# Kernel optimization log

Measured on AMD Instinct MI355X. Metric: run time of the kernel, lower is better.

## Reference

```python
import jax, jax.numpy as jnp
import numpy as np
import math

B = 2; SEQ = 4096; D_MODEL = 768; D_STATE = 128; D_CONV = 4; EXPAND = 2; HEAD_DIM = 64
D_INNER = EXPAND * D_MODEL; D_SSM = D_INNER; NH = D_SSM // HEAD_DIM  # 24 heads
CONV_DIM = D_SSM + 2 * D_STATE; CHUNK = 256
D_IN_PROJ = 2 * D_INNER + 2 * D_STATE + NH


def causal_conv1d(x, w, b):
    # x: [B, C, L]; w: [C, W] depthwise kernel; left-pad for causality; silu activation
    W = w.shape[-1]; L = x.shape[-1]
    xp = jnp.pad(x, ((0, 0), (0, 0), (W - 1, 0)))
    y = b[None, :, None] + sum(xp[:, :, k:k + L] * w[None, :, k, None] for k in range(W))
    return jax.nn.silu(y)


def segsum(a):
    # a: [..., S] -> [..., S, S]; entry (i,j) = sum_{k=j+1..i} a_k for i>=j, -inf above diag
    S = a.shape[-1]
    cs = jnp.cumsum(a, -1)
    d = cs[..., :, None] - cs[..., None, :]
    mask = jnp.tril(jnp.ones((S, S), bool))
    return jnp.where(mask, d, -jnp.inf)


def ssd_chunk_scan(x, dt, A, Bm, Cm, Dp, chunk):
    # Mamba2 SSD chunked selective scan. x:[b,l,h,p] dt:[b,l,h] A:[h] Bm,Cm:[b,l,n] Dp:[h]
    b, l, h, p = x.shape; n = Bm.shape[-1]; nc = l // chunk
    xc = x.reshape(b, nc, chunk, h, p)
    Bc = Bm.reshape(b, nc, chunk, n)
    Cc = Cm.reshape(b, nc, chunk, n)
    dtc = dt.reshape(b, nc, chunk, h)
    a = jnp.transpose(A[None, None, None, :] * dtc, (0, 3, 1, 2))  # [b,h,c,s]
    Acs = jnp.cumsum(a, -1)
    Lm = jnp.exp(segsum(a))  # [b,h,c,s,s] lower-triangular decay
    # intra-chunk (diagonal block) outputs
    Ydiag = jnp.einsum('bcsn,bczn,bhcsz,bczh,bczhp->bcshp', Cc, Bc, Lm, dtc, xc)
    # per-chunk end states
    decay_states = jnp.exp(Acs[..., -1:] - Acs)  # [b,h,c,s]
    states = jnp.einsum('bczn,bhcz,bczh,bczhp->bchpn', Bc, decay_states, dtc, xc)
    # inter-chunk recurrence over nc chunks (small) via scan
    decay_chunk = jnp.exp(Acs[..., -1])  # [b,h,c]
    def step(hcar, inp):
        dcy, st = inp
        return dcy[..., None, None] * hcar + st, hcar  # emit state entering chunk
    _, prev = jax.lax.scan(step, jnp.zeros_like(states[:, 0]),
                           (jnp.moveaxis(decay_chunk, -1, 0), jnp.moveaxis(states, 1, 0)))
    prev = jnp.moveaxis(prev, 0, 1)  # [b,c,h,p,n]
    Yoff = jnp.einsum('bcsn,bchpn,bhcs->bcshp', Cc, prev, jnp.exp(Acs))
    return (Ydiag + Yoff).reshape(b, l, h, p) + Dp[None, None, :, None] * x


def _forward(u, time_diff, W_in, b_in, conv_w, conv_b, tconv1_w, tconv1_b,
             tconv2_w, tconv2_b, mlp_w1, mlp_b1, mlp_w2, mlp_b2, gate_w, gate_b,
             ln_w, ln_b, A_log, dt_bias, Dp, norm_w, W_out, b_out):
    silu = jax.nn.silu
    zxbcdt = u @ W_in.T + b_in  # [B,L,d_in_proj], d_mlp=0
    z = zxbcdt[..., :D_SSM]
    xBC = zxbcdt[..., D_SSM:D_SSM + CONV_DIM]
    dt = zxbcdt[..., D_SSM + CONV_DIM:]  # [B,L,H]
    A = -jnp.exp(A_log)
    xBC = jnp.transpose(causal_conv1d(jnp.transpose(xBC, (0, 2, 1)), conv_w, conv_b), (0, 2, 1))
    # time-gated dt path (time_diff: [B,H,L])
    ts = silu(time_diff @ mlp_w1.T + mlp_b1) @ mlp_w2.T + mlp_b2
    tdt = ts * time_diff
    tdt = causal_conv1d(tdt, tconv1_w, tconv1_b)
    tdt = causal_conv1d(tdt, tconv2_w, tconv2_b)  # [B,H,L]
    final_dt = dt * jnp.transpose(tdt, (0, 2, 1))
    x = xBC[..., :D_SSM]
    Bm = xBC[..., D_SSM:D_SSM + D_STATE]
    Cm = xBC[..., D_SSM + D_STATE:]
    dt_sp = jax.nn.softplus(final_dt + dt_bias)
    xh = x.reshape(x.shape[0], x.shape[1], NH, HEAD_DIM)
    y = ssd_chunk_scan(xh, dt_sp, A, Bm, Cm, Dp, CHUNK).reshape(x.shape[0], x.shape[1], D_SSM)
    # gated RMSNorm (norm_before_gate=False): gate first, then normalize
    yg = y * silu(z)
    y = yg * jax.lax.rsqrt(jnp.mean(yg * yg, -1, keepdims=True) + 1e-12) * norm_w
    out = y @ W_out.T + b_out
    # time residual gate + LayerNorm over seq_len
    tg = jax.nn.sigmoid(time_diff @ gate_w.T + gate_b)  # [B,H,1]
    tmix = tg * time_diff + (1.0 - tg) * tdt
    mu = jnp.mean(tmix, -1, keepdims=True)
    var = jnp.mean((tmix - mu) ** 2, -1, keepdims=True)
    time_out = (tmix - mu) * jax.lax.rsqrt(var + 1e-12) * ln_w + ln_b
    return out, time_out


def setup_inputs():
    key = jax.random.key(0)
    ks = jax.random.split(key, 16)
    def nrm(k, shape, scale=0.02):
        return jax.random.normal(k, shape, jnp.float32) * scale
    dtv = jnp.exp(jax.random.uniform(ks[10], (NH,), jnp.float32) * (math.log(0.1) - math.log(0.001)) + math.log(0.001))
    dtv = jnp.clip(dtv, 1e-4)
    dt_bias = dtv + jnp.log(-jnp.expm1(-dtv))
    A_log = jnp.log(jax.random.uniform(ks[11], (NH,), jnp.float32, 1.0, 16.0))
    return dict(
        u=jax.random.normal(ks[0], (B, SEQ, D_MODEL), jnp.float32),
        time_diff=jax.random.uniform(ks[1], (B, NH, SEQ), jnp.float32),
        W_in=nrm(ks[2], (D_IN_PROJ, D_MODEL)), b_in=jnp.zeros((D_IN_PROJ,), jnp.float32),
        conv_w=nrm(ks[3], (CONV_DIM, D_CONV), 0.2), conv_b=jnp.zeros((CONV_DIM,), jnp.float32),
        tconv1_w=nrm(ks[4], (NH, D_CONV), 0.2), tconv1_b=jnp.zeros((NH,), jnp.float32),
        tconv2_w=nrm(ks[5], (NH, D_CONV), 0.2), tconv2_b=jnp.zeros((NH,), jnp.float32),
        mlp_w1=nrm(ks[6], (SEQ, SEQ)), mlp_b1=jnp.zeros((SEQ,), jnp.float32),
        mlp_w2=nrm(ks[7], (SEQ, SEQ)), mlp_b2=jnp.zeros((SEQ,), jnp.float32),
        gate_w=nrm(ks[8], (1, SEQ)), gate_b=jnp.zeros((1,), jnp.float32),
        ln_w=jnp.ones((SEQ,), jnp.float32), ln_b=jnp.zeros((SEQ,), jnp.float32),
        A_log=A_log, dt_bias=dt_bias, Dp=jnp.ones((NH,), jnp.float32),
        norm_w=jnp.ones((D_SSM,), jnp.float32),
        W_out=nrm(ks[9], (D_MODEL, D_INNER)), b_out=jnp.zeros((D_MODEL,), jnp.float32),
    )


def reference(u, time_diff, W_in, b_in, conv_w, conv_b, tconv1_w, tconv1_b,
              tconv2_w, tconv2_b, mlp_w1, mlp_b1, mlp_w2, mlp_b2, gate_w, gate_b,
              ln_w, ln_b, A_log, dt_bias, Dp, norm_w, W_out, b_out):
    return _forward(u, time_diff, W_in, b_in, conv_w, conv_b, tconv1_w, tconv1_b,
                    tconv2_w, tconv2_b, mlp_w1, mlp_b1, mlp_w2, mlp_b2, gate_w, gate_b,
                    ln_w, ln_b, A_log, dt_bias, Dp, norm_w, W_out, b_out)
```

## Files before the change

### kernel.cpp

```cpp
#include <hip/hip_runtime.h>
#include <math.h>

#define BB 2
#define SEQ 4096
#define DMODEL 768
#define DSTATE 128
#define NHH 24
#define HDIM 64
#define DSSM 1536
#define CDIM 1792
#define CHK 256
#define NC 16
#define DPROJ 3352
#define MR (BB*SEQ)
#define KSPLIT 32
#define XSTR 1920
#define CT 16
#define SXS 270
#define STS 134

typedef __attribute__((ext_vector_type(8))) short bf16x8;
typedef __attribute__((ext_vector_type(8))) unsigned short u16x8;
typedef __attribute__((ext_vector_type(4))) float f32x4;

__device__ __forceinline__ float siluf(float x) { return x / (1.0f + expf(-x)); }

__device__ __forceinline__ unsigned short f2bf(float f) {
    unsigned u = __float_as_uint(f);
    unsigned r = (u + 0x7fffu + ((u >> 16) & 1u)) >> 16;
    return (unsigned short)r;
}

__device__ __forceinline__ float bf2f(unsigned short u) {
    return __uint_as_float(((unsigned)u) << 16);
}

__device__ __forceinline__ float4 bf2f4(ushort4 v) {
    float4 o;
    o.x = bf2f(v.x); o.y = bf2f(v.y); o.z = bf2f(v.z); o.w = bf2f(v.w);
    return o;
}

__device__ __forceinline__ bf16x8 pack8(float4 a, float4 b) {
    u16x8 r;
    r[0] = f2bf(a.x); r[1] = f2bf(a.y); r[2] = f2bf(a.z); r[3] = f2bf(a.w);
    r[4] = f2bf(b.x); r[5] = f2bf(b.y); r[6] = f2bf(b.z); r[7] = f2bf(b.w);
    return *(bf16x8*)&r;
}

__device__ __forceinline__ void gload_lds16(const void* g, void* l) {
    __builtin_amdgcn_global_load_lds((const __attribute__((address_space(1))) unsigned int*)g,
                                     (__attribute__((address_space(3))) unsigned int*)l, 16, 0, 0);
}

__global__ __launch_bounds__(256) void cvt_bf16_k(const float* __restrict__ in,
    unsigned short* __restrict__ out, int n_valid, int n_total)
{
    int i = (blockIdx.x * 256 + threadIdx.x) * 4;
    if (i >= n_total) return;
    ushort4 o;
    if (i + 3 < n_valid) {
        float4 v = *(const float4*)&in[i];
        o.x = f2bf(v.x); o.y = f2bf(v.y); o.z = f2bf(v.z); o.w = f2bf(v.w);
    } else {
        o.x = (i + 0 < n_valid) ? f2bf(in[i + 0]) : 0;
        o.y = (i + 1 < n_valid) ? f2bf(in[i + 1]) : 0;
        o.z = (i + 2 < n_valid) ? f2bf(in[i + 2]) : 0;
        o.w = (i + 3 < n_valid) ? f2bf(in[i + 3]) : 0;
    }
    *(ushort4*)&out[i] = o;
}

__global__ __launch_bounds__(256) void gemm_mfma_dual(
    const unsigned short* __restrict__ A,
    const unsigned short* __restrict__ B1, const float* __restrict__ bias1,
    unsigned short* __restrict__ C1, int N1, int NT1, int nbias1, int NWG1,
    const unsigned short* __restrict__ B2, const float* __restrict__ bias2,
    unsigned short* __restrict__ C2, int N2, int NT2, int nbias2,
    int K, int KT)
{
    __shared__ unsigned short SMEM[24576];
    const int tid = threadIdx.x;
    const int w = tid >> 6, l = tid & 63;
    const int wr = w >> 1, wc = w & 1;
    const int lr = l & 15, lk = l >> 4;
    const int lkx = lk ^ ((lr >> 1) & 3);
    int nwg = gridDim.x, bid = blockIdx.x;
    int wg = (nwg & 7) ? bid : ((bid & 7) * (nwg >> 3) + (bid >> 3));
    const unsigned short* B;
    const float* bias;
    unsigned short* C;
    int N, NT, nbias;
    if (wg < NWG1) { B = B1; bias = bias1; C = C1; N = N1; NT = NT1; nbias = nbias1; }
    else { wg -= NWG1; B = B2; bias = bias2; C = C2; N = N2; NT = NT2; nbias = nbias2; }
    const int m0 = (wg / NT) * 128, n0 = (wg % NT) * 128;
    f32x4 acc[4][4] = {};
    const int i16 = w * 64 + l;
    const int row0 = i16 >> 2, sl = i16 & 3;
    const int slx = sl ^ ((row0 >> 1) & 3);
    const size_t ga0 = (size_t)(m0 + row0) * K + slx * 8;
    const size_t ga1 = (size_t)(m0 + row0 + 64) * K + slx * 8;
    const size_t gb0 = (size_t)(n0 + row0) * K + slx * 8;
    const size_t gb1 = (size_t)(n0 + row0 + 64) * K + slx * 8;
    const int lo0 = (w * 64) * 8;
    const int lo1 = (256 + w * 64) * 8;

#define STAGE(bb, kt) { int ko = (kt) * 32; int bs = (bb) * 8192;            \
      gload_lds16(A + ga0 + ko, &SMEM[bs + lo0]);                            \
      gload_lds16(A + ga1 + ko, &SMEM[bs + lo1]);                            \
      gload_lds16(B + gb0 + ko, &SMEM[bs + 4096 + lo0]);                     \
      gload_lds16(B + gb1 + ko, &SMEM[bs + 4096 + lo1]); }

    STAGE(0, 0);
    STAGE(1, 1);
    for (int kt = 0; kt < KT; ++kt) {
        if (kt + 1 < KT) {
            asm volatile("s_waitcnt vmcnt(4)" ::: "memory");
        } else {
            asm volatile("s_waitcnt vmcnt(0)" ::: "memory");
        }
        __builtin_amdgcn_s_barrier();
        if (kt + 2 < KT) STAGE((kt + 2) % 3, kt + 2);
        int bs = (kt % 3) * 8192;
        bf16x8 af[4], bg[4];
#pragma unroll
        for (int mi = 0; mi < 4; ++mi)
            af[mi] = *(const bf16x8*)&SMEM[bs + (wr * 64 + mi * 16 + lr) * 32 + lkx * 8];
#pragma unroll
        for (int nj = 0; nj < 4; ++nj)
            bg[nj] = *(const bf16x8*)&SMEM[bs + 4096 + (wc * 64 + nj * 16 + lr) * 32 + lkx * 8];
#pragma unroll
        for (int mi = 0; mi < 4; ++mi)
#pragma unroll
            for (int nj = 0; nj < 4; ++nj)
                acc[mi][nj] = __builtin_amdgcn_mfma_f32_16x16x32_bf16(af[mi], bg[nj], acc[mi][nj], 0, 0, 0);
    }
#undef STAGE
    {
        unsigned short* CL = SMEM;
#pragma unroll
        for (int half = 0; half < 2; ++half) {
            __syncthreads();
            if (wr == half) {
#pragma unroll
                for (int nj = 0; nj < 4; ++nj) {
                    int col = n0 + wc * 64 + nj * 16 + lr;
                    float bz = (col < nbias) ? bias[col] : 0.f;
                    int cl = wc * 64 + nj * 16 + lr;
#pragma unroll
                    for (int mi = 0; mi < 4; ++mi)
#pragma unroll
                        for (int r = 0; r < 4; ++r)
                            CL[(mi * 16 + lk * 4 + r) * 136 + cl] = f2bf(acc[mi][nj][r] + bz);
                }
            }
            __syncthreads();
            for (int i = tid; i < 1024; i += 256) {
                int rr = i >> 4, c8 = (i & 15) * 8;
                int m = m0 + half * 64 + rr;
                *(u16x8*)&C[(size_t)m * N + n0 + c8] = *(const u16x8*)&CL[rr * 136 + c8];
            }
        }
    }
}

__global__ __launch_bounds__(256) void gemm_skinny_mfma(const float* __restrict__ A,
    const float* __restrict__ Bw, float* __restrict__ part, int N, int K)
{
    const int nb = blockIdx.x, kb = blockIdx.y;
    const int n0 = nb * 128;
    const int KS = K / KSPLIT;
    const int k0 = kb * KS;
    const int tid = threadIdx.x;
    const int w = tid >> 6, l = tid & 63;
    const int lr = l & 15, lk = l >> 4;
    const int nw0 = n0 + w * 32;
    f32x4 acc[3][2] = {};
    for (int kt = 0; kt < KS; kt += 32) {
        int kk = k0 + kt + lk * 8;
        bf16x8 af[3], bfr[2];
#pragma unroll
        for (int mi = 0; mi < 3; ++mi) {
            const float* ap = &A[(size_t)(mi * 16 + lr) * K + kk];
            af[mi] = pack8(*(const float4*)ap, *(const float4*)(ap + 4));
        }
#pragma unroll
        for (int nf = 0; nf < 2; ++nf) {
            const float* bp = &Bw[(size_t)(nw0 + nf * 16 + lr) * K + kk];
            bfr[nf] = pack8(*(const float4*)bp, *(const float4*)(bp + 4));
        }
#pragma unroll
        for (int mi = 0; mi < 3; ++mi)
#pragma unroll
            for (int nf = 0; nf < 2; ++nf)
                acc[mi][nf] = __builtin_amdgcn_mfma_f32_16x16x32_bf16(af[mi], bfr[nf], acc[mi][nf], 0, 0, 0);
    }
    float* pb = part + (size_t)kb * 48 * N;
#pragma unroll
    for (int mi = 0; mi < 3; ++mi)
#pragma unroll
        for (int r = 0; r < 4; ++r)
#pragma unroll
            for (int nf = 0; nf < 2; ++nf)
                pb[(size_t)(mi * 16 + lk * 4 + r) * N + nw0 + nf * 16 + lr] = acc[mi][nf][r];
}

__global__ __launch_bounds__(256) void conv_xbc_k(const unsigned short* __restrict__ xbc,
    const float* __restrict__ cw, const float* __restrict__ cb,
    unsigned short* __restrict__ out)
{
    int idx = blockIdx.x * 256 + threadIdx.x;
    if (idx >= 448 * (MR / CT)) return;
    int slot = idx % 448;
    int g = idx / 448;
    int c4 = slot * 4;
    int b = g / (SEQ / CT);
    int t0 = (g % (SEQ / CT)) * CT;
    size_t rb = (size_t)b * SEQ;
    float4 cw0 = *(const float4*)&cw[(c4 + 0) * 4];
    float4 cw1 = *(const float4*)&cw[(c4 + 1) * 4];
    float4 cw2 = *(const float4*)&cw[(c4 + 2) * 4];
    float4 cw3 = *(const float4*)&cw[(c4 + 3) * 4];
    float4 cbv = *(const float4*)&cb[c4];
    float4 zero = {0.f, 0.f, 0.f, 0.f};
    float4 w0, w1, w2;
    w0 = (t0 - 3 >= 0) ? bf2f4(*(const ushort4*)&xbc[(rb + t0 - 3) * XSTR + c4]) : zero;
    w1 = (t0 - 2 >= 0) ? bf2f4(*(const ushort4*)&xbc[(rb + t0 - 2) * XSTR + c4]) : zero;
    w2 = (t0 - 1 >= 0) ? bf2f4(*(const ushort4*)&xbc[(rb + t0 - 1) * XSTR + c4]) : zero;
#pragma unroll
    for (int i = 0; i < CT; ++i) {
        int t = t0 + i;
        float4 w3 = bf2f4(*(const ushort4*)&xbc[(rb + t) * XSTR + c4]);
        float a0 = cbv.x + w0.x * cw0.x + w1.x * cw0.y + w2.x * cw0.z + w3.x * cw0.w;
        float a1 = cbv.y + w0.y * cw1.x + w1.y * cw1.y + w2.y * cw1.z + w3.y * cw1.w;
        float a2 = cbv.z + w0.z * cw2.x + w1.z * cw2.y + w2.z * cw2.z + w3.z * cw2.w;
        float a3 = cbv.w + w0.w * cw3.x + w1.w * cw3.y + w2.w * cw3.z + w3.w * cw3.w;
        ushort4 o;
        o.x = f2bf(siluf(a0)); o.y = f2bf(siluf(a1));
        o.z = f2bf(siluf(a2)); o.w = f2bf(siluf(a3));
        *(ushort4*)&out[(rb + t) * CDIM + c4] = o;
        w0 = w1; w1 = w2; w2 = w3;
    }
}

__global__ __launch_bounds__(256) void reduce_part_k(const float* __restrict__ part,
    const float* __restrict__ bias, float* __restrict__ out, int N, int act)
{
    int idx = blockIdx.x * 256 + threadIdx.x;
    if (idx >= 48 * N) return;
    int n = idx % N;
    float s = bias[n];
#pragma unroll
    for (int kb = 0; kb < KSPLIT; ++kb) s += part[(size_t)kb * 48 * N + idx];
    if (act) s = siluf(s);
    out[idx] = s;
}

__global__ __launch_bounds__(256) void time_conv_k(const float* __restrict__ ts,
    const float* __restrict__ td, const float* __restrict__ w1, const float* __restrict__ b1,
    const float* __restrict__ w2, const float* __restrict__ b2, float* __restrict__ tdt)
{
    __shared__ float u0[SEQ];
    __shared__ float u1[SEQ];
    int row = blockIdx.x, h = row % NHH;
    const float* tsr = ts + (size_t)row * SEQ;
    const float* tdr = td + (size_t)row * SEQ;
    for (int i = threadIdx.x; i < SEQ; i += 256) u0[i] = tsr[i] * tdr[i];
    __syncthreads();
    float wa[4], wb[4];
#pragma unroll
    for (int k = 0; k < 4; ++k) { wa[k] = w1[h * 4 + k]; wb[k] = w2[h * 4 + k]; }
    float ba = b1[h], bbv = b2[h];
    for (int i = threadIdx.x; i < SEQ; i += 256) {
        float acc = ba;
#pragma unroll
        for (int k = 0; k < 4; ++k) { int tt = i + k - 3; if (tt >= 0) acc = fmaf(u0[tt], wa[k], acc); }
        u1[i] = siluf(acc);
    }
    __syncthreads();
    for (int i = threadIdx.x; i < SEQ; i += 256) {
        float acc = bbv;
#pragma unroll
        for (int k = 0; k < 4; ++k) { int tt = i + k - 3; if (tt >= 0) acc = fmaf(u1[tt], wb[k], acc); }
        tdt[(size_t)row * SEQ + i] = siluf(acc);
    }
}

__global__ __launch_bounds__(256) void dtsp_cum_k(const unsigned short* __restrict__ r1,
    const float* __restrict__ tdt, const float* __restrict__ dt_bias,
    const float* __restrict__ A_log, float* __restrict__ dtp, float* __restrict__ acs)
{
    __shared__ float wsum[4];
    int blk = blockIdx.x;
    int c = blk % NC;
    int bh = blk / NC;
    int h = bh % NHH, b = bh / NHH;
    int tid = threadIdx.x;
    int s = c * CHK + tid;
    size_t base = (size_t)bh * SEQ + s;
    float x = bf2f(r1[((size_t)(b * SEQ + s)) * XSTR + CDIM + h]) * tdt[base] + dt_bias[h];
    float dt = (x > 20.0f) ? x : log1pf(expf(x));
    dtp[base] = dt;
    float Ah = -expf(A_log[h]);
    float v = Ah * dt;
    int ln = tid & 63;
#pragma unroll
    for (int off = 1; off < 64; off <<= 1) {
        float t = __shfl_up(v, off, 64);
        if (ln >= off) v += t;
    }
    if (ln == 63) wsum[tid >> 6] = v;
    __syncthreads();
    float add = 0.f;
    int wv = tid >> 6;
#pragma unroll
    for (int i = 0; i < 3; ++i)
        if (i < wv) add += wsum[i];
    acs[base] = v + add;
}

__global__ __launch_bounds__(256) void ssd_states_sraw_k(const unsigned short* __restrict__ xc,
    const float* __restrict__ dtp, const float* __restrict__ acs_g,
    float* __restrict__ st, unsigned short* __restrict__ sraw)
{
    __shared__ float s_coef[256];
    __shared__ unsigned short SXT[64 * STS];
    __shared__ unsigned short SBT[128 * STS];
    int bid = blockIdx.x;
    int blk = (gridDim.x & 7) ? bid : ((bid & 7) * (gridDim.x >> 3) + (bid >> 3));
    int tid = threadIdx.x;
    int w = tid >> 6, l = tid & 63;
    int lr = l & 15, lk = l >> 4;
    if (blk >= BB * NC * NHH) {
        int t = blk - BB * NC * NHH;
        int bc = t / 10, tile = t % 10;
        int rem = tile, st_i = 0;
        for (st_i = 0; ; ++st_i) { if (rem < st_i + 1) break; rem -= st_i + 1; }
        int zt = rem;
        int b = bc / NC, c = bc % NC;
        size_t rowbase = (size_t)b * SEQ + c * CHK;
        for (int i = tid; i < 64 * 32; i += 256) {
            int r = i >> 5, c4 = (i & 31) * 4;
            *(ushort4*)&SXT[r * STS + c4] = *(const ushort4*)&xc[(rowbase + st_i * 64 + r) * CDIM + DSSM + DSTATE + c4];
            *(ushort4*)&SBT[r * STS + c4] = *(const ushort4*)&xc[(rowbase + zt * 64 + r) * CDIM + DSSM + c4];
        }
        __syncthreads();
        f32x4 d[4] = {};
#pragma unroll
        for (int kt = 0; kt < 4; ++kt) {
            bf16x8 av = *(const bf16x8*)&SXT[(w * 16 + lr) * STS + kt * 32 + lk * 8];
            bf16x8 bv[4];
#pragma unroll
            for (int nj = 0; nj < 4; ++nj)
                bv[nj] = *(const bf16x8*)&SBT[(nj * 16 + lr) * STS + kt * 32 + lk * 8];
#pragma unroll
            for (int nj = 0; nj < 4; ++nj)
                d[nj] = __builtin_amdgcn_mfma_f32_16x16x32_bf16(av, bv[nj], d[nj], 0, 0, 0);
        }
        unsigned short* tp = sraw + (size_t)bc * 16 * 4096 + (size_t)(st_i * 4 + zt) * 4096;
#pragma unroll
        for (int nj = 0; nj < 4; ++nj)
#pragma unroll
            for (int r = 0; r < 4; ++r)
                tp[(w * 16 + lk * 4 + r) * 64 + nj * 16 + lr] = f2bf(d[nj][r]);
        return;
    }
    int h = blk % NHH, c = (blk / NHH) % NC, b = blk / (NHH * NC);
    size_t rowbase = (size_t)b * SEQ + c * CHK;
    size_t dbase = (size_t)(b * NHH + h) * SEQ + c * CHK;
    float alv = acs_g[dbase + 255];
    s_coef[tid] = expf(alv - acs_g[dbase + tid]) * dtp[dbase + tid];
    __syncthreads();
    f32x4 acc[4][2] = {};
    for (int z0 = 0; z0 < CHK; z0 += 128) {
        if (z0) __syncthreads();
        for (int i = tid; i < 128 * 8; i += 256) {
            int zz = i >> 3, p8 = (i & 7) * 8;
            float sc = s_coef[z0 + zz];
            u16x8 v = *(const u16x8*)&xc[(rowbase + z0 + zz) * CDIM + h * HDIM + p8];
#pragma unroll
            for (int e = 0; e < 8; ++e)
                SXT[(p8 + e) * STS + zz] = f2bf(bf2f(v[e]) * sc);
        }
        for (int i = tid; i < 128 * 16; i += 256) {
            int zz = i >> 4, n8 = (i & 15) * 8;
            u16x8 v = *(const u16x8*)&xc[(rowbase + z0 + zz) * CDIM + DSSM + n8];
#pragma unroll
            for (int e = 0; e < 8; ++e)
                SBT[(n8 + e) * STS + zz] = v[e];
        }
        __syncthreads();
#pragma unroll
        for (int kt = 0; kt < 4; ++kt) {
            bf16x8 av[4], bv[2];
#pragma unroll
            for (int mi = 0; mi < 4; ++mi)
                av[mi] = *(const bf16x8*)&SXT[(mi * 16 + lr) * STS + kt * 32 + lk * 8];
#pragma unroll
            for (int nj = 0; nj < 2; ++nj)
                bv[nj] = *(const bf16x8*)&SBT[(w * 32 + nj * 16 + lr) * STS + kt * 32 + lk * 8];
#pragma unroll
            for (int mi = 0; mi < 4; ++mi)
#pragma unroll
                for (int nj = 0; nj < 2; ++nj)
                    acc[mi][nj] = __builtin_amdgcn_mfma_f32_16x16x32_bf16(av[mi], bv[nj], acc[mi][nj], 0, 0, 0);
        }
    }
    size_t base = (size_t)blk * (HDIM * DSTATE);
#pragma unroll
    for (int mi = 0; mi < 4; ++mi)
#pragma unroll
        for (int r = 0; r < 4; ++r) {
            int p = mi * 16 + lk * 4 + r;
#pragma unroll
            for (int nj = 0; nj < 2; ++nj)
                st[base + p * DSTATE + w * 32 + nj * 16 + lr] = acc[mi][nj][r];
        }
}

__global__ __launch_bounds__(256) void ssd_scan_k(const float* __restrict__ st,
    const float* __restrict__ acs_g, unsigned short* __restrict__ pv16)
{
    int b = blockIdx.x / NHH, h = blockIdx.x % NHH;
    int tid = threadIdx.x;
    float carry[32];
#pragma unroll
    for (int j = 0; j < 32; ++j) carry[j] = 0.f;
    for (int c = 0; c < NC; ++c) {
        int bch = (b * NC + c) * NHH + h;
        size_t base = (size_t)bch * (HDIM * DSTATE);
        float dcy = expf(acs_g[(size_t)(b * NHH + h) * SEQ + c * CHK + 255]);
#pragma unroll
        for (int j = 0; j < 32; ++j) {
            pv16[base + tid + j * 256] = f2bf(carry[j]);
            carry[j] = fmaf(dcy, carry[j], st[base + tid + j * 256]);
        }
    }
}

__global__ __launch_bounds__(256) void ssd_y2_k(const unsigned short* __restrict__ xc,
    const float* __restrict__ dtp, const float* __restrict__ acs_g,
    const unsigned short* __restrict__ sraw, const unsigned short* __restrict__ pv16,
    const float* __restrict__ Dp, unsigned short* __restrict__ Ybf)
{
    __shared__ unsigned short SXT[32 * SXS];
    int bid = blockIdx.x;
    int blk2 = (gridDim.x & 7) ? bid : ((bid & 7) * (gridDim.x >> 3) + (bid >> 3));
    int half = blk2 & 1;
    int blk = blk2 >> 1;
    int h = blk % NHH;
    int c = (blk / NHH) % NC;
    int b = blk / (NHH * NC);
    int tid = threadIdx.x;
    int w = tid >> 6, l = tid & 63;
    int lr = l & 15, lk = l >> 4;
    int pbase = half * 32;
    size_t rowbase = (size_t)b * SEQ + c * CHK;
    size_t dbase = (size_t)(b * NHH + h) * SEQ + c * CHK;
    for (int i = tid; i < 256 * 4; i += 256) {
        int z = i >> 2, p8 = (i & 3) * 8;
        float az0q = acs_g[dbase + (z & 192)];
        float e = az0q - acs_g[dbase + z];
        if (e > 60.f) e = 60.f;
        float sc = expf(e) * dtp[dbase + z];
        u16x8 v = *(const u16x8*)&xc[(rowbase + z) * CDIM + h * HDIM + pbase + p8];
#pragma unroll
        for (int e2 = 0; e2 < 8; ++e2)
            SXT[(p8 + e2) * SXS + z] = f2bf(bf2f(v[e2]) * sc);
    }
    float az0w = acs_g[dbase + w * 64];
    float esw[4][4];
#pragma unroll
    for (int mi = 0; mi < 4; ++mi)
#pragma unroll
        for (int r = 0; r < 4; ++r)
            esw[mi][r] = expf(acs_g[dbase + w * 64 + mi * 16 + lk * 4 + r] - az0w);
    __syncthreads();

    const unsigned short* tbase = sraw + (size_t)(b * NC + c) * 16 * 4096;
    const unsigned short* pvbase = pv16 + (size_t)blk * (HDIM * DSTATE);
    f32x4 acc[4][2] = {};
    for (int zt = 0; zt < w; ++zt) {
        const unsigned short* tp = tbase + (size_t)(w * 4 + zt) * 4096;
        f32x4 tmp[4][2] = {};
#pragma unroll
        for (int kt = 0; kt < 2; ++kt) {
            bf16x8 av[4], bv[2];
#pragma unroll
            for (int mi = 0; mi < 4; ++mi)
                av[mi] = *(const bf16x8*)&tp[(mi * 16 + lr) * 64 + kt * 32 + lk * 8];
#pragma unroll
            for (int nj = 0; nj < 2; ++nj)
                bv[nj] = *(const bf16x8*)&SXT[(nj * 16 + lr) * SXS + zt * 64 + kt * 32 + lk * 8];
#pragma unroll
            for (int mi = 0; mi < 4; ++mi)
#pragma unroll
                for (int nj = 0; nj < 2; ++nj)
                    tmp[mi][nj] = __builtin_amdgcn_mfma_f32_16x16x32_bf16(av[mi], bv[nj], tmp[mi][nj], 0, 0, 0);
        }
        float rho = expf(az0w - acs_g[dbase + zt * 64]);
#pragma unroll
        for (int mi = 0; mi < 4; ++mi)
#pragma unroll
            for (int r = 0; r < 4; ++r) {
                float es = esw[mi][r] * rho;
#pragma unroll
                for (int nj = 0; nj < 2; ++nj)
                    acc[mi][nj][r] += es * tmp[mi][nj][r];
            }
    }
    {
        const unsigned short* tp = tbase + (size_t)(w * 4 + w) * 4096;
        f32x4 tmp[4][2] = {};
#pragma unroll
        for (int kt = 0; kt < 2; ++kt) {
            bf16x8 av[4], bv[2];
#pragma unroll
            for (int mi = 0; mi < 4; ++mi) {
                av[mi] = *(const bf16x8*)&tp[(mi * 16 + lr) * 64 + kt * 32 + lk * 8];
                int zb = kt * 32 + lk * 8;
                int sl = mi * 16 + lr;
#pragma unroll
                for (int e = 0; e < 8; ++e)
                    if (zb + e > sl) av[mi][e] = 0;
            }
#pragma unroll
            for (int nj = 0; nj < 2; ++nj)
                bv[nj] = *(const bf16x8*)&SXT[(nj * 16 + lr) * SXS + w * 64 + kt * 32 + lk * 8];
#pragma unroll
            for (int mi = 0; mi < 4; ++mi)
#pragma unroll
                for (int nj = 0; nj < 2; ++nj)
                    tmp[mi][nj] = __builtin_amdgcn_mfma_f32_16x16x32_bf16(av[mi], bv[nj], tmp[mi][nj], 0, 0, 0);
        }
#pragma unroll
        for (int mi = 0; mi < 4; ++mi)
#pragma unroll
            for (int r = 0; r < 4; ++r) {
                float es = esw[mi][r];
#pragma unroll
                for (int nj = 0; nj < 2; ++nj)
                    acc[mi][nj][r] += es * tmp[mi][nj][r];
            }
    }
    {
        f32x4 tmp[4][2] = {};
#pragma unroll
        for (int kt = 0; kt < 4; ++kt) {
            bf16x8 av[4], bv[2];
#pragma unroll
            for (int mi = 0; mi < 4; ++mi)
                av[mi] = *(const bf16x8*)&xc[(rowbase + w * 64 + mi * 16 + lr) * CDIM + DSSM + DSTATE + kt * 32 + lk * 8];
#pragma unroll
            for (int nj = 0; nj < 2; ++nj)
                bv[nj] = *(const bf16x8*)&pvbase[(pbase + nj * 16 + lr) * DSTATE + kt * 32 + lk * 8];
#pragma unroll
            for (int mi = 0; mi < 4; ++mi)
#pragma unroll
                for (int nj = 0; nj < 2; ++nj)
                    tmp[mi][nj] = __builtin_amdgcn_mfma_f32_16x16x32_bf16(av[mi], bv[nj], tmp[mi][nj], 0, 0, 0);
        }
        float eoff = expf(az0w);
#pragma unroll
        for (int mi = 0; mi < 4; ++mi)
#pragma unroll
            for (int r = 0; r < 4; ++r) {
                float es = esw[mi][r] * eoff;
#pragma unroll
                for (int nj = 0; nj < 2; ++nj)
                    acc[mi][nj][r] += es * tmp[mi][nj][r];
            }
    }
    float dph = Dp[h];
#pragma unroll
    for (int mi = 0; mi < 4; ++mi) {
#pragma unroll
        for (int r = 0; r < 4; ++r) {
            int s = w * 64 + mi * 16 + lk * 4 + r;
#pragma unroll
            for (int nj = 0; nj < 2; ++nj) {
                int p = pbase + nj * 16 + lr;
                float xv = bf2f(xc[(rowbase + s) * CDIM + h * HDIM + p]);
                Ybf[(rowbase + s) * DSSM + h * HDIM + p] = f2bf(acc[mi][nj][r] + dph * xv);
            }
        }
    }
}

__global__ __launch_bounds__(256) void rmsnorm_k(const unsigned short* __restrict__ Ybf_in,
    const unsigned short* __restrict__ zbf, const float* __restrict__ nw,
    unsigned short* __restrict__ Ybf_out)
{
    __shared__ float red[8];
    int row = blockIdx.x;
    const unsigned short* y = Ybf_in + (size_t)row * DSSM;
    const unsigned short* z = zbf + (size_t)row * DSSM;
    float v[6];
    float ss = 0.f;
#pragma unroll
    for (int k = 0; k < 6; ++k) {
        int i = threadIdx.x + k * 256;
        float g = bf2f(y[i]) * siluf(bf2f(z[i]));
        v[k] = g;
        ss = fmaf(g, g, ss);
    }
#pragma unroll
    for (int o = 32; o > 0; o >>= 1) ss += __shfl_down(ss, o, 64);
    int wv = threadIdx.x >> 6, ln = threadIdx.x & 63;
    if (ln == 0) red[wv] = ss;
    __syncthreads();
    float tot = red[0] + red[1] + red[2] + red[3];
    float sc = rsqrtf(tot / (float)DSSM + 1e-12f);
    unsigned short* yo = Ybf_out + (size_t)row * DSSM;
#pragma unroll
    for (int k = 0; k < 6; ++k) {
        int i = threadIdx.x + k * 256;
        yo[i] = f2bf(v[k] * sc * nw[i]);
    }
}

__global__ __launch_bounds__(256) void gemm_out_timeout_k(
    const unsigned short* __restrict__ A, const unsigned short* __restrict__ B,
    const float* __restrict__ bias, float* __restrict__ C, int N, int K, int KT, int NT, int NWGG,
    const float* __restrict__ td, const float* __restrict__ tdt,
    const float* __restrict__ gw, const float* __restrict__ gb,
    const float* __restrict__ lnw, const float* __restrict__ lnb, float* __restrict__ out2)
{
    __shared__ __align__(16) unsigned char SMEMRAW[49152];
    unsigned short* SMEM = (unsigned short*)SMEMRAW;
    const int tid = threadIdx.x;
    int nwg = gridDim.x, bid = blockIdx.x;
    int wg = (nwg & 7) ? bid : ((bid & 7) * (nwg >> 3) + (bid >> 3));
    if (wg >= NWGG) {
        float* tm = (float*)SMEMRAW;
        __shared__ float red[8];
        int row = wg - NWGG;
        const float* tdr = td + (size_t)row * SEQ;
        const float* tdtr = tdt + (size_t)row * SEQ;
        int wv = tid >> 6, ln = tid & 63;
        float part = 0.f;
        for (int i = tid; i < SEQ; i += 256) part = fmaf(tdr[i], gw[i], part);
#pragma unroll
        for (int o = 32; o > 0; o >>= 1) part += __shfl_down(part, o, 64);
        if (ln == 0) red[wv] = part;
        __syncthreads();
        float dot = red[0] + red[1] + red[2] + red[3];
        float tg = 1.f / (1.f + expf(-(dot + gb[0])));
        __syncthreads();
        float sum = 0.f;
        for (int i = tid; i < SEQ; i += 256) {
            float x = tg * tdr[i] + (1.f - tg) * tdtr[i];
            tm[i] = x;
            sum += x;
        }
#pragma unroll
        for (int o = 32; o > 0; o >>= 1) sum += __shfl_down(sum, o, 64);
        if (ln == 0) red[wv] = sum;
        __syncthreads();
        float mu = (red[0] + red[1] + red[2] + red[3]) / (float)SEQ;
        __syncthreads();
        float s2 = 0.f;
        for (int i = tid; i < SEQ; i += 256) { float d = tm[i] - mu; s2 = fmaf(d, d, s2); }
#pragma unroll
        for (int o = 32; o > 0; o >>= 1) s2 += __shfl_down(s2, o, 64);
        if (ln == 0) red[wv] = s2;
        __syncthreads();
        float var = (red[0] + red[1] + red[2] + red[3]) / (float)SEQ;
        float inv = rsqrtf(var + 1e-12f);
        for (int i = tid; i < SEQ; i += 256)
            out2[(size_t)row * SEQ + i] = (tm[i] - mu) * inv * lnw[i] + lnb[i];
        return;
    }
    const int w = tid >> 6, l = tid & 63;
    const int wr = w >> 1, wc = w & 1;
    const int lr = l & 15, lk = l >> 4;
    const int lkx = lk ^ ((lr >> 1) & 3);
    const int m0 = (wg / NT) * 128, n0 = (wg % NT) * 128;
    f32x4 acc[4][4] = {};
    const int i16 = w * 64 + l;
    const int row0 = i16 >> 2, sl = i16 & 3;
    const int slx = sl ^ ((row0 >> 1) & 3);
    const size_t ga0 = (size_t)(m0 + row0) * K + slx * 8;
    const size_t ga1 = (size_t)(m0 + row0 + 64) * K + slx * 8;
    const size_t gb0 = (size_t)(n0 + row0) * K + slx * 8;
    const size_t gb1 = (size_t)(n0 + row0 + 64) * K + slx * 8;
    const int lo0 = (w * 64) * 8;
    const int lo1 = (256 + w * 64) * 8;

#define STAGE3(bb, kt) { int ko = (kt) * 32; int bs = (bb) * 8192;           \
      gload_lds16(A + ga0 + ko, &SMEM[bs + lo0]);                            \
      gload_lds16(A + ga1 + ko, &SMEM[bs + lo1]);                            \
      gload_lds16(B + gb0 + ko, &SMEM[bs + 4096 + lo0]);                     \
      gload_lds16(B + gb1 + ko, &SMEM[bs + 4096 + lo1]); }

    STAGE3(0, 0);
    STAGE3(1, 1);
    for (int kt = 0; kt < KT; ++kt) {
        if (kt + 1 < KT) {
            asm volatile("s_waitcnt vmcnt(4)" ::: "memory");
        } else {
            asm volatile("s_waitcnt vmcnt(0)" ::: "memory");
        }
        __builtin_amdgcn_s_barrier();
        if (kt + 2 < KT) STAGE3((kt + 2) % 3, kt + 2);
        int bs = (kt % 3) * 8192;
        bf16x8 af[4], bg[4];
#pragma unroll
        for (int mi = 0; mi < 4; ++mi)
            af[mi] = *(const bf16x8*)&SMEM[bs + (wr * 64 + mi * 16 + lr) * 32 + lkx * 8];
#pragma unroll
        for (int nj = 0; nj < 4; ++nj)
            bg[nj] = *(const bf16x8*)&SMEM[bs + 4096 + (wc * 64 + nj * 16 + lr) * 32 + lkx * 8];
#pragma unroll
        for (int mi = 0; mi < 4; ++mi)
#pragma unroll
            for (int nj = 0; nj < 4; ++nj)
                acc[mi][nj] = __builtin_amdgcn_mfma_f32_16x16x32_bf16(af[mi], bg[nj], acc[mi][nj], 0, 0, 0);
    }
#undef STAGE3
#pragma unroll
    for (int nj = 0; nj < 4; ++nj) {
        int col = n0 + wc * 64 + nj * 16 + lr;
        float bz = bias[col];
#pragma unroll
        for (int mi = 0; mi < 4; ++mi) {
#pragma unroll
            for (int r = 0; r < 4; ++r) {
                int m = m0 + wr * 64 + mi * 16 + lk * 4 + r;
                C[(size_t)m * N + col] = acc[mi][nj][r] + bz;
            }
        }
    }
}

extern "C" void kernel_launch(void* const* d_in, const int* in_sizes, int n_in,
                              void* d_out, int out_size, void* d_ws, size_t ws_size,
                              hipStream_t stream)
{
    const float* u      = (const float*)d_in[0];
    const float* td     = (const float*)d_in[1];
    const float* W_in   = (const float*)d_in[2];
    const float* b_in   = (const float*)d_in[3];
    const float* conv_w = (const float*)d_in[4];
    const float* conv_b = (const float*)d_in[5];
    const float* t1w    = (const float*)d_in[6];
    const float* t1b    = (const float*)d_in[7];
    const float* t2w    = (const float*)d_in[8];
    const float* t2b    = (const float*)d_in[9];
    const float* m1w    = (const float*)d_in[10];
    const float* m1b    = (const float*)d_in[11];
    const float* m2w    = (const float*)d_in[12];
    const float* m2b    = (const float*)d_in[13];
    const float* gw     = (const float*)d_in[14];
    const float* gb     = (const float*)d_in[15];
    const float* lnw    = (const float*)d_in[16];
    const float* lnb    = (const float*)d_in[17];
    const float* A_log  = (const float*)d_in[18];
    const float* dt_bias= (const float*)d_in[19];
    const float* Dpv    = (const float*)d_in[20];
    const float* nw     = (const float*)d_in[21];
    const float* W_out  = (const float*)d_in[22];
    const float* b_out  = (const float*)d_in[23];
    float* out  = (float*)d_out;
    float* out2 = out + (size_t)MR * DMODEL;

    float* ws = (float*)d_ws;
    size_t o = 0;
    float* zbuf  = ws + o; o += (size_t)MR * DSSM;
    float* r1    = ws + o; o += (size_t)MR * DSSM;
    float* xcv   = ws + o; o += (size_t)MR * CDIM / 2;
    float* partb = ws + o; o += (size_t)KSPLIT * 48 * SEQ;
    float* hid   = ws + o; o += (size_t)BB * NHH * SEQ;
    float* tss   = ws + o; o += (size_t)BB * NHH * SEQ;
    float* tdt   = ws + o; o += (size_t)BB * NHH * SEQ;
    float* dtp   = ws + o; o += (size_t)MR * NHH;
    float* acs_g = ws + o; o += (size_t)MR * NHH;
    float* pvb   = ws + o; o += (size_t)BB * NC * NHH * HDIM * DSTATE;
    unsigned short* sraw = (unsigned short*)(ws + o); o += (size_t)BB * NC * 16 * 4096 / 2;
    unsigned short* r1b = (unsigned short*)r1;
    float* stb = r1;
    unsigned short* ybf16 = (unsigned short*)r1;
    unsigned short* xcv_bf = (unsigned short*)xcv;
    unsigned short* u_bf  = (unsigned short*)pvb;
    unsigned short* Wi_bf = (unsigned short*)(pvb + 3145728);
    unsigned short* pv16  = (unsigned short*)pvb;
    unsigned short* zbf   = (unsigned short*)zbuf;
    unsigned short* Y_bf  = (unsigned short*)xcv;
    unsigned short* Wo_bf = (unsigned short*)(zbuf + 6291456);

    dim3 blk(256);
    const int NWG1 = (XSTR / 128) * (MR / 128);

    cvt_bf16_k<<<dim3((MR * DMODEL / 4 + 255) / 256), blk, 0, stream>>>(u, u_bf, MR * DMODEL, MR * DMODEL);
    cvt_bf16_k<<<dim3((3456 * DMODEL / 4 + 255) / 256), blk, 0, stream>>>(W_in, Wi_bf, DPROJ * DMODEL, 3456 * DMODEL);
    cvt_bf16_k<<<dim3((DMODEL * DSSM / 4 + 255) / 256), blk, 0, stream>>>(W_out, Wo_bf, DMODEL * DSSM, DMODEL * DSSM);
    gemm_skinny_mfma<<<dim3(SEQ / 128, KSPLIT), blk, 0, stream>>>(td, m1w, partb, SEQ, SEQ);
    gemm_mfma_dual<<<dim3(NWG1 + (DSSM / 128) * (MR / 128)), blk, 0, stream>>>(
        u_bf,
        Wi_bf + (size_t)DSSM * DMODEL, b_in + DSSM, r1b, XSTR, XSTR / 128, DPROJ - DSSM, NWG1,
        Wi_bf, b_in, zbf, DSSM, DSSM / 128, DSSM,
        DMODEL, DMODEL / 32);
    reduce_part_k<<<dim3((48 * SEQ + 255) / 256), blk, 0, stream>>>(partb, m1b, hid, SEQ, 1);
    gemm_skinny_mfma<<<dim3(SEQ / 128, KSPLIT), blk, 0, stream>>>(hid, m2w, partb, SEQ, SEQ);
    conv_xbc_k<<<dim3((448 * (MR / CT) + 255) / 256), blk, 0, stream>>>(r1b, conv_w, conv_b, xcv_bf);
    reduce_part_k<<<dim3((48 * SEQ + 255) / 256), blk, 0, stream>>>(partb, m2b, tss, SEQ, 0);
    time_conv_k<<<dim3(BB * NHH), blk, 0, stream>>>(tss, td, t1w, t1b, t2w, t2b, tdt);
    dtsp_cum_k<<<dim3(BB * NHH * NC), blk, 0, stream>>>(r1b, tdt, dt_bias, A_log, dtp, acs_g);
    ssd_states_sraw_k<<<dim3(BB * NC * NHH + BB * NC * 10), blk, 0, stream>>>(xcv_bf, dtp, acs_g, stb, sraw);
    ssd_scan_k<<<dim3(BB * NHH), blk, 0, stream>>>(stb, acs_g, pv16);
    ssd_y2_k<<<dim3(BB * NC * NHH * 2), blk, 0, stream>>>(xcv_bf, dtp, acs_g, sraw, pv16, Dpv, ybf16);
    rmsnorm_k<<<dim3(MR), blk, 0, stream>>>(ybf16, zbf, nw, Y_bf);
    gemm_out_timeout_k<<<dim3((DMODEL / 128) * (MR / 128) + BB * NHH), blk, 0, stream>>>(
        Y_bf, Wo_bf, b_out, out, DMODEL, DSSM, DSSM / 32, DMODEL / 128, (DMODEL / 128) * (MR / 128),
        td, tdt, gw, gb, lnw, lnb, out2);
}
```

Before: 328.9 us.

## Merge skinny time-MLP GEMMs into the in-proj GEMM and conv launches

The first skinny split-K MLP GEMM now runs as extra workgroups appended to the dual in-proj GEMM grid, and the second skinny GEMM runs as extra workgroups in the causal-conv launch. Each workgroup branches on its block index to pick its role. This removes two kernel launches and lets independent small work fill idle compute units alongside the larger kernels. In exchange, the merged kernels carry more code and registers, which could lower occupancy. The block-index remapping also now spans the combined grid, so GEMM tile ordering may change.

Result: no change. 325.8 us (-0.9%).

```diff
diff --git a/kernel.cpp b/kernel.cpp
--- a/kernel.cpp
+++ b/kernel.cpp
@@ -71,22 +71,61 @@
     *(ushort4*)&out[i] = o;
 }
 
-__global__ __launch_bounds__(256) void gemm_mfma_dual(
+__global__ __launch_bounds__(256) void gemm_dual_skinny(
     const unsigned short* __restrict__ A,
     const unsigned short* __restrict__ B1, const float* __restrict__ bias1,
     unsigned short* __restrict__ C1, int N1, int NT1, int nbias1, int NWG1,
     const unsigned short* __restrict__ B2, const float* __restrict__ bias2,
     unsigned short* __restrict__ C2, int N2, int NT2, int nbias2,
-    int K, int KT)
+    int K, int KT, int NWGD,
+    const float* __restrict__ skA, const float* __restrict__ skB,
+    float* __restrict__ skPart, int skN, int skK)
 {
     __shared__ unsigned short SMEM[24576];
     const int tid = threadIdx.x;
     const int w = tid >> 6, l = tid & 63;
-    const int wr = w >> 1, wc = w & 1;
     const int lr = l & 15, lk = l >> 4;
-    const int lkx = lk ^ ((lr >> 1) & 3);
     int nwg = gridDim.x, bid = blockIdx.x;
     int wg = (nwg & 7) ? bid : ((bid & 7) * (nwg >> 3) + (bid >> 3));
+    if (wg >= NWGD) {
+        int t = wg - NWGD;
+        int nb = t & 31, kb = t >> 5;
+        const int n0s = nb * 128;
+        const int KS = skK / KSPLIT;
+        const int k0 = kb * KS;
+        const int nw0 = n0s + w * 32;
+        f32x4 sacc[3][2] = {};
+        for (int kt = 0; kt < KS; kt += 32) {
+            int kk = k0 + kt + lk * 8;
+            bf16x8 af[3], bfr[2];
+#pragma unroll
+            for (int mi = 0; mi < 3; ++mi) {
+                const float* ap = &skA[(size_t)(mi * 16 + lr) * skK + kk];
+                af[mi] = pack8(*(const float4*)ap, *(const float4*)(ap + 4));
+            }
+#pragma unroll
+            for (int nf = 0; nf < 2; ++nf) {
+                const float* bp = &skB[(size_t)(nw0 + nf * 16 + lr) * skK + kk];
+                bfr[nf] = pack8(*(const float4*)bp, *(const float4*)(bp + 4));
+            }
+#pragma unroll
+            for (int mi = 0; mi < 3; ++mi)
+#pragma unroll
+                for (int nf = 0; nf < 2; ++nf)
+                    sacc[mi][nf] = __builtin_amdgcn_mfma_f32_16x16x32_bf16(af[mi], bfr[nf], sacc[mi][nf], 0, 0, 0);
+        }
+        float* pb = skPart + (size_t)kb * 48 * skN;
+#pragma unroll
+        for (int mi = 0; mi < 3; ++mi)
+#pragma unroll
+            for (int r = 0; r < 4; ++r)
+#pragma unroll
+                for (int nf = 0; nf < 2; ++nf)
+                    pb[(size_t)(mi * 16 + lk * 4 + r) * skN + nw0 + nf * 16 + lr] = sacc[mi][nf][r];
+        return;
+    }
+    const int wr = w >> 1, wc = w & 1;
+    const int lkx = lk ^ ((lr >> 1) & 3);
     const unsigned short* B;
     const float* bias;
     unsigned short* C;
@@ -164,53 +203,54 @@
     }
 }
 
-__global__ __launch_bounds__(256) void gemm_skinny_mfma(const float* __restrict__ A,
-    const float* __restrict__ Bw, float* __restrict__ part, int N, int K)
-{
-    const int nb = blockIdx.x, kb = blockIdx.y;
-    const int n0 = nb * 128;
-    const int KS = K / KSPLIT;
-    const int k0 = kb * KS;
-    const int tid = threadIdx.x;
-    const int w = tid >> 6, l = tid & 63;
-    const int lr = l & 15, lk = l >> 4;
-    const int nw0 = n0 + w * 32;
-    f32x4 acc[3][2] = {};
-    for (int kt = 0; kt < KS; kt += 32) {
-        int kk = k0 + kt + lk * 8;
-        bf16x8 af[3], bfr[2];
-#pragma unroll
-        for (int mi = 0; mi < 3; ++mi) {
-            const float* ap = &A[(size_t)(mi * 16 + lr) * K + kk];
-            af[mi] = pack8(*(const float4*)ap, *(const float4*)(ap + 4));
-        }
-#pragma unroll
-        for (int nf = 0; nf < 2; ++nf) {
-            const float* bp = &Bw[(size_t)(nw0 + nf * 16 + lr) * K + kk];
-            bfr[nf] = pack8(*(const float4*)bp, *(const float4*)(bp + 4));
-        }
+__global__ __launch_bounds__(256) void conv_skinny2_k(const unsigned short* __restrict__ xbc,
+    const float* __restrict__ cw, const float* __restrict__ cb,
+    unsigned short* __restrict__ out,
+    const float* __restrict__ skA, const float* __restrict__ skB,
+    float* __restrict__ skPart, int skN, int skK, int NWGC)
+{
+    int bid = blockIdx.x;
+    int tid = threadIdx.x;
+    if (bid >= NWGC) {
+        int t = bid - NWGC;
+        int nb = t & 31, kb = t >> 5;
+        const int n0s = nb * 128;
+        const int KS = skK / KSPLIT;
+        const int k0 = kb * KS;
+        const int w = tid >> 6, l = tid & 63;
+        const int lr = l & 15, lk = l >> 4;
+        const int nw0 = n0s + w * 32;
+        f32x4 sacc[3][2] = {};
+        for (int kt = 0; kt < KS; kt += 32) {
+            int kk = k0 + kt + lk * 8;
+            bf16x8 af[3], bfr[2];
+#pragma unroll
+            for (int mi = 0; mi < 3; ++mi) {
+                const float* ap = &skA[(size_t)(mi * 16 + lr) * skK + kk];
+                af[mi] = pack8(*(const float4*)ap, *(const float4*)(ap + 4));
+            }
+#pragma unroll
+            for (int nf = 0; nf < 2; ++nf) {
+                const float* bp = &skB[(size_t)(nw0 + nf * 16 + lr) * skK + kk];
+                bfr[nf] = pack8(*(const float4*)bp, *(const float4*)(bp + 4));
+            }
+#pragma unroll
+            for (int mi = 0; mi < 3; ++mi)
+#pragma unroll
+                for (int nf = 0; nf < 2; ++nf)
+                    sacc[mi][nf] = __builtin_amdgcn_mfma_f32_16x16x32_bf16(af[mi], bfr[nf], sacc[mi][nf], 0, 0, 0);
+        }
+        float* pb = skPart + (size_t)kb * 48 * skN;
 #pragma unroll
         for (int mi = 0; mi < 3; ++mi)
 #pragma unroll
-            for (int nf = 0; nf < 2; ++nf)
-                acc[mi][nf] = __builtin_amdgcn_mfma_f32_16x16x32_bf16(af[mi], bfr[nf], acc[mi][nf], 0, 0, 0);
-    }
-    float* pb = part + (size_t)kb * 48 * N;
-#pragma unroll
-    for (int mi = 0; mi < 3; ++mi)
-#pragma unroll
-        for (int r = 0; r < 4; ++r)
-#pragma unroll
-            for (int nf = 0; nf < 2; ++nf)
-                pb[(size_t)(mi * 16 + lk * 4 + r) * N + nw0 + nf * 16 + lr] = acc[mi][nf][r];
-}
-
-__global__ __launch_bounds__(256) void conv_xbc_k(const unsigned short* __restrict__ xbc,
-    const float* __restrict__ cw, const float* __restrict__ cb,
-    unsigned short* __restrict__ out)
-{
-    int idx = blockIdx.x * 256 + threadIdx.x;
-    if (idx >= 448 * (MR / CT)) return;
+            for (int r = 0; r < 4; ++r)
+#pragma unroll
+                for (int nf = 0; nf < 2; ++nf)
+                    pb[(size_t)(mi * 16 + lk * 4 + r) * skN + nw0 + nf * 16 + lr] = sacc[mi][nf][r];
+        return;
+    }
+    int idx = bid * 256 + tid;
     int slot = idx % 448;
     int g = idx / 448;
     int c4 = slot * 4;
@@ -790,19 +830,22 @@
 
     dim3 blk(256);
     const int NWG1 = (XSTR / 128) * (MR / 128);
+    const int NWGD = NWG1 + (DSSM / 128) * (MR / 128);
+    const int NWGSK = (SEQ / 128) * KSPLIT;
+    const int NWGC = 448 * (MR / CT) / 256;
 
     cvt_bf16_k<<<dim3((MR * DMODEL / 4 + 255) / 256), blk, 0, stream>>>(u, u_bf, MR * DMODEL, MR * DMODEL);
     cvt_bf16_k<<<dim3((3456 * DMODEL / 4 + 255) / 256), blk, 0, stream>>>(W_in, Wi_bf, DPROJ * DMODEL, 3456 * DMODEL);
     cvt_bf16_k<<<dim3((DMODEL * DSSM / 4 + 255) / 256), blk, 0, stream>>>(W_out, Wo_bf, DMODEL * DSSM, DMODEL * DSSM);
-    gemm_skinny_mfma<<<dim3(SEQ / 128, KSPLIT), blk, 0, stream>>>(td, m1w, partb, SEQ, SEQ);
-    gemm_mfma_dual<<<dim3(NWG1 + (DSSM / 128) * (MR / 128)), blk, 0, stream>>>(
+    gemm_dual_skinny<<<dim3(NWGD + NWGSK), blk, 0, stream>>>(
         u_bf,
         Wi_bf + (size_t)DSSM * DMODEL, b_in + DSSM, r1b, XSTR, XSTR / 128, DPROJ - DSSM, NWG1,
         Wi_bf, b_in, zbf, DSSM, DSSM / 128, DSSM,
-        DMODEL, DMODEL / 32);
+        DMODEL, DMODEL / 32, NWGD,
+        td, m1w, partb, SEQ, SEQ);
     reduce_part_k<<<dim3((48 * SEQ + 255) / 256), blk, 0, stream>>>(partb, m1b, hid, SEQ, 1);
-    gemm_skinny_mfma<<<dim3(SEQ / 128, KSPLIT), blk, 0, stream>>>(hid, m2w, partb, SEQ, SEQ);
-    conv_xbc_k<<<dim3((448 * (MR / CT) + 255) / 256), blk, 0, stream>>>(r1b, conv_w, conv_b, xcv_bf);
+    conv_skinny2_k<<<dim3(NWGC + NWGSK), blk, 0, stream>>>(
+        r1b, conv_w, conv_b, xcv_bf, hid, m2w, partb, SEQ, SEQ, NWGC);
     reduce_part_k<<<dim3((48 * SEQ + 255) / 256), blk, 0, stream>>>(partb, m2b, tss, SEQ, 0);
     time_conv_k<<<dim3(BB * NHH), blk, 0, stream>>>(tss, td, t1w, t1b, t2w, t2b, tdt);
     dtsp_cum_k<<<dim3(BB * NHH * NC), blk, 0, stream>>>(r1b, tdt, dt_bias, A_log, dtp, acs_g);
```
